# Kernel tuning notes

Measured on AMD Instinct MI355X. Metric: run time of the kernel, lower is better.

The kernel has to match this reference:

```python
import jax, jax.numpy as jnp
import numpy as np

DIM = 128  # matches init kwarg `dim`; scale = 1/sqrt(dim)


def setup_inputs() -> dict:
    key = jax.random.key(0)
    kq, kk, kv = jax.random.split(key, 3)
    B, S, D = 16, 2048, 128
    return {
        "query": jax.random.normal(kq, (B, S, D), dtype=jnp.float32),
        "key": jax.random.normal(kk, (B, S, D), dtype=jnp.float32),
        "value": jax.random.normal(kv, (B, S, D), dtype=jnp.float32),
    }


def reference(query, key, value):
    # scores = Q K^T / sqrt(dim)  -> [B, S, S]
    scale = 1.0 / np.sqrt(DIM).astype(np.float32)
    scores = jnp.einsum("bqd,bkd->bqk", query, key) * scale
    attn = jax.nn.softmax(scores, axis=-1)
    # context = attn @ V -> [B, S, D]
    return jnp.einsum("bqk,bkd->bqd", attn, value)
```

## Files before the change

### kernel.cpp

```cpp
#include <hip/hip_runtime.h>
#include <hip/hip_bf16.h>

namespace {

constexpr int kS  = 2048;
constexpr int kD  = 128;
constexpr int kKB = 64;
constexpr int kNT = kS / kKB;
constexpr int kTileUS = 1024 * 8;
constexpr size_t kImgUShorts = (size_t)16 * 32 * kTileUS;

typedef __attribute__((ext_vector_type(8)))  short bf16x8;
typedef __attribute__((ext_vector_type(16))) float f32x16;
typedef __attribute__((ext_vector_type(4)))  unsigned int u32x4;

__device__ inline unsigned short f2bf(float f) {
  return __builtin_bit_cast(unsigned short, __float2bfloat16(f));
}
__device__ inline unsigned pk2(float lo, float hi) {
  return (unsigned)f2bf(lo) | ((unsigned)f2bf(hi) << 16);
}
__device__ inline float fexp2(float x) { return __builtin_amdgcn_exp2f(x); }

__device__ inline void gload_lds16(const void* g, void* l) {
  __builtin_amdgcn_global_load_lds(
      (const __attribute__((address_space(1))) unsigned int*)g,
      (__attribute__((address_space(3))) unsigned int*)l, 16, 0, 0);
}

__global__ __launch_bounds__(256)
void convert_kv(const float* __restrict__ K, const float* __restrict__ V,
                unsigned short* __restrict__ Kws, unsigned short* __restrict__ Vws)
{
  const int tid = threadIdx.x;
  const int gid = blockIdx.x & 511;
  const int b = gid >> 5, t = gid & 31;
  if (blockIdx.x < 512) {
    const float* src = K + ((size_t)b * kS + t * kKB) * kD;
    unsigned short* dst = Kws + (size_t)gid * kTileUS;
#pragma unroll
    for (int i = 0; i < 4; ++i) {
      const int CH = i * 256 + tid;
      const int k = CH >> 4, s = CH & 15;
      const int d8 = s ^ (k & 15);
      const float* p = src + (size_t)k * kD + d8 * 8;
      float4 a = *reinterpret_cast<const float4*>(p);
      float4 c = *reinterpret_cast<const float4*>(p + 4);
      bf16x8 o;
      o[0] = (short)f2bf(a.x); o[1] = (short)f2bf(a.y);
      o[2] = (short)f2bf(a.z); o[3] = (short)f2bf(a.w);
      o[4] = (short)f2bf(c.x); o[5] = (short)f2bf(c.y);
      o[6] = (short)f2bf(c.z); o[7] = (short)f2bf(c.w);
      *reinterpret_cast<bf16x8*>(dst + (size_t)CH * 8) = o;
    }
  } else {
    __shared__ unsigned short VT[128 * 72];
    const float* src = V + ((size_t)b * kS + t * kKB) * kD;
#pragma unroll
    for (int i = 0; i < 8; ++i) {
      const int idx = i * 256 + tid;
      const int k = idx >> 5, d4 = idx & 31;
      float4 v = *reinterpret_cast<const float4*>(src + (size_t)k * kD + d4 * 4);
      VT[(d4 * 4 + 0) * 72 + k] = f2bf(v.x);
      VT[(d4 * 4 + 1) * 72 + k] = f2bf(v.y);
      VT[(d4 * 4 + 2) * 72 + k] = f2bf(v.z);
      VT[(d4 * 4 + 3) * 72 + k] = f2bf(v.w);
    }
    __syncthreads();
    unsigned short* dst = Vws + (size_t)gid * kTileUS;
#pragma unroll
    for (int i = 0; i < 4; ++i) {
      const int CH = i * 256 + tid;
      const int d = CH >> 3, s = CH & 7;
      const int k8 = s ^ (d & 7);
      bf16x8 v = *reinterpret_cast<const bf16x8*>(&VT[d * 72 + k8 * 8]);
      *reinterpret_cast<bf16x8*>(dst + (size_t)CH * 8) = v;
    }
  }
}

__global__ __launch_bounds__(256, 2)
void attn_fwd(const float* __restrict__ Q,
              const unsigned short* __restrict__ Kws,
              const unsigned short* __restrict__ Vws,
              float* __restrict__ O)
{
  __shared__ __align__(16) unsigned char smem[65536];
  __shared__ float mls[2 * 2 * 32];

  const int tid  = threadIdx.x;
  const int wv   = tid >> 6;
  const int qg   = wv >> 1;
  const int ksp  = wv & 1;
  const int lane = tid & 63;
  const int l31  = lane & 31;
  const int hi   = lane >> 5;
  const int m15  = l31 & 15;
  const int m7   = l31 & 7;

  const int bid   = blockIdx.x;
  const int xcd   = bid & 7;
  const int slot  = bid >> 3;
  const int batch = xcd * 2 + (slot >> 5);
  const int qt    = slot & 31;

  const float* Qb = Q + (size_t)batch * kS * kD;
  float*       Ob = O + (size_t)batch * kS * kD;
  const int qrow0 = qt * 64 + qg * 32;

  auto stageK = [&](int t, int buf) {
    const unsigned short* src = Kws + (size_t)(batch * 32 + t) * kTileUS + (wv * 256 + lane) * 8;
    unsigned char* kd = smem + buf * 16384 + wv * 4096;
    gload_lds16(src,            kd);
    gload_lds16(src + 64 * 8,   kd + 1024);
    gload_lds16(src + 128 * 8,  kd + 2048);
    gload_lds16(src + 192 * 8,  kd + 3072);
  };
  auto stageV = [&](int t, int buf) {
    const unsigned short* src = Vws + (size_t)(batch * 32 + t) * kTileUS + (wv * 256 + lane) * 8;
    unsigned char* vd = smem + 32768 + buf * 16384 + wv * 4096;
    gload_lds16(src,            vd);
    gload_lds16(src + 64 * 8,   vd + 1024);
    gload_lds16(src + 128 * 8,  vd + 2048);
    gload_lds16(src + 192 * 8,  vd + 3072);
  };

  stageK(0, 0); stageV(0, 0); stageK(1, 1);

  constexpr float kQScale = 0.08838834764831845f * 1.4426950408889634f;
  bf16x8 qf[8];
#pragma unroll
  for (int c = 0; c < 8; ++c) {
    const float* p = Qb + (size_t)(qrow0 + l31) * kD + c * 16 + hi * 8;
    float4 a = *reinterpret_cast<const float4*>(p);
    float4 b = *reinterpret_cast<const float4*>(p + 4);
    bf16x8 f;
    f[0] = (short)f2bf(a.x * kQScale); f[1] = (short)f2bf(a.y * kQScale);
    f[2] = (short)f2bf(a.z * kQScale); f[3] = (short)f2bf(a.w * kQScale);
    f[4] = (short)f2bf(b.x * kQScale); f[5] = (short)f2bf(b.y * kQScale);
    f[6] = (short)f2bf(b.z * kQScale); f[7] = (short)f2bf(b.w * kQScale);
    qf[c] = f;
  }

  f32x16 acc[4];
#pragma unroll
  for (int dt = 0; dt < 4; ++dt)
#pragma unroll
    for (int r = 0; r < 16; ++r) acc[dt][r] = 0.f;
  float mrun = -1e30f, lrun = 0.f;
  bf16x8 pa0, pa1;

  __syncthreads();

  const unsigned short* Ksm = reinterpret_cast<const unsigned short*>(smem);
  const unsigned short* Vsm = reinterpret_cast<const unsigned short*>(smem + 32768);
  const int kRowBase = (ksp * 32 + l31) * 128;

  auto qk = [&](int kb) -> f32x16 {
    f32x16 sc;
#pragma unroll
    for (int r = 0; r < 16; ++r) sc[r] = 0.f;
    __builtin_amdgcn_s_setprio(1);
#pragma unroll
    for (int c = 0; c < 8; ++c) {
      const int s = ((c << 1) | hi) ^ m15;
      bf16x8 kf = *reinterpret_cast<const bf16x8*>(&Ksm[kb * 8192 + kRowBase + s * 8]);
      sc = __builtin_amdgcn_mfma_f32_32x32x16_bf16(kf, qf[c], sc, 0, 0, 0);
    }
    __builtin_amdgcn_s_setprio(0);
    return sc;
  };
  auto treemax = [&](const f32x16& sc) {
    float m0 = sc[0];
#pragma unroll
    for (int r = 1; r < 16; ++r) m0 = fmaxf(m0, sc[r]);
    return fmaxf(m0, __shfl_xor(m0, 32));
  };
  auto pv = [&](int vb) {
    const int o0 = (ksp << 2) | hi;
    __builtin_amdgcn_s_setprio(1);
#pragma unroll
    for (int dt = 0; dt < 4; ++dt) {
      const int vRow = vb * 8192 + (dt * 32 + l31) * 64;
      bf16x8 vf0 = *reinterpret_cast<const bf16x8*>(&Vsm[vRow + (o0 ^ m7) * 8]);
      acc[dt] = __builtin_amdgcn_mfma_f32_32x32x16_bf16(vf0, pa0, acc[dt], 0, 0, 0);
      bf16x8 vf1 = *reinterpret_cast<const bf16x8*>(&Vsm[vRow + ((o0 ^ 2) ^ m7) * 8]);
      acc[dt] = __builtin_amdgcn_mfma_f32_32x32x16_bf16(vf1, pa1, acc[dt], 0, 0, 0);
    }
    __builtin_amdgcn_s_setprio(0);
  };
  auto pack = [&](const f32x16& p) {
    unsigned a0 = pk2(p[0], p[1]),   a1 = pk2(p[2],  p[3]);
    unsigned a2 = pk2(p[4], p[5]),   a3 = pk2(p[6],  p[7]);
    unsigned b0 = pk2(p[8], p[9]),   b1 = pk2(p[10], p[11]);
    unsigned b2 = pk2(p[12], p[13]), b3 = pk2(p[14], p[15]);
    asm("v_permlane32_swap_b32 %0, %1" : "+v"(a0), "+v"(a2));
    asm("v_permlane32_swap_b32 %0, %1" : "+v"(a1), "+v"(a3));
    asm("v_permlane32_swap_b32 %0, %1" : "+v"(b0), "+v"(b2));
    asm("v_permlane32_swap_b32 %0, %1" : "+v"(b1), "+v"(b3));
    u32x4 w0 = {a0, a1, a2, a3};
    u32x4 w1 = {b0, b1, b2, b3};
    pa0 = __builtin_bit_cast(bf16x8, w0);
    pa1 = __builtin_bit_cast(bf16x8, w1);
  };

  {
    f32x16 sc = qk(0);
    mrun = treemax(sc);
    float rs = 0.f;
#pragma unroll
    for (int r = 0; r < 16; ++r) { sc[r] = fexp2(sc[r] - mrun); rs += sc[r]; }
    rs += __shfl_xor(rs, 32);
    lrun = rs;
    pack(sc);
  }
  __syncthreads();

  for (int t = 0; t < kNT - 1; ++t) {
    const int kb = (t + 1) & 1, vb = t & 1;
    if (t + 2 < kNT) stageK(t + 2, vb);
    stageV(t + 1, kb);

    f32x16 sc = qk(kb);
    const float mt = treemax(sc);
    const bool need = !__all(mt - mrun <= 8.0f);
    const float mnew = need ? fmaxf(mrun, mt) : mrun;

    pv(vb);

    float rs = 0.f;
#pragma unroll
    for (int r = 0; r < 16; ++r) { sc[r] = fexp2(sc[r] - mnew); rs += sc[r]; }
    rs += __shfl_xor(rs, 32);
    if (need) {
      const float corr = fexp2(mrun - mnew);
      lrun *= corr;
#pragma unroll
      for (int dt = 0; dt < 4; ++dt)
#pragma unroll
        for (int r = 0; r < 16; ++r) acc[dt][r] *= corr;
    }
    lrun += rs;
    mrun = mnew;
    pack(sc);

    __syncthreads();
  }

  pv((kNT - 1) & 1);
  __syncthreads();

  float* scr = reinterpret_cast<float*>(smem);
  auto scrAt = [&](int reg, int q, int d) -> float& {
    return scr[reg * 4096 + q * 128 + (d ^ ((q & 7) << 2))];
  };
  auto drow = [&](int r) { return (r & 3) + 8 * (r >> 2) + 4 * hi; };

  if (ksp == 1) {
#pragma unroll
    for (int dt = 0; dt < 4; ++dt)
#pragma unroll
      for (int r = 0; r < 16; ++r)
        scrAt(qg, l31, dt * 32 + drow(r)) = acc[dt][r];
    mls[(qg * 2 + 0) * 32 + l31] = mrun;
    mls[(qg * 2 + 1) * 32 + l31] = lrun;
  }
  __syncthreads();
  if (ksp == 0) {
    const float m2 = mls[(qg * 2 + 0) * 32 + l31];
    const float l2 = mls[(qg * 2 + 1) * 32 + l31];
    const float mm = fmaxf(mrun, m2);
    const float w1 = fexp2(mrun - mm), w2 = fexp2(m2 - mm);
    const float inv = 1.0f / (lrun * w1 + l2 * w2);
#pragma unroll
    for (int dt = 0; dt < 4; ++dt)
#pragma unroll
      for (int r = 0; r < 16; ++r) {
        const int d = dt * 32 + drow(r);
        float o1 = scrAt(qg, l31, d);
        scrAt(qg, l31, d) = (acc[dt][r] * w1 + o1 * w2) * inv;
      }
  }
  __syncthreads();
  const int krow = tid >> 5, c4 = tid & 31;
#pragma unroll
  for (int i = 0; i < 8; ++i) {
    const int row = i * 8 + krow;
    const int q = row & 31;
    float4 val = *reinterpret_cast<const float4*>(
        &scr[(row >> 5) * 4096 + q * 128 + ((c4 * 4) ^ ((q & 7) << 2))]);
    *reinterpret_cast<float4*>(&Ob[(size_t)(qt * 64 + row) * kD + c4 * 4]) = val;
  }
}

}

extern "C" void kernel_launch(void* const* d_in, const int* in_sizes, int n_in,
                              void* d_out, int out_size, void* d_ws, size_t ws_size,
                              hipStream_t stream) {
  const float* Q = (const float*)d_in[0];
  const float* K = (const float*)d_in[1];
  const float* V = (const float*)d_in[2];
  float* O = (float*)d_out;
  (void)in_sizes; (void)n_in; (void)out_size; (void)ws_size;

  unsigned short* Kws = (unsigned short*)d_ws;
  unsigned short* Vws = Kws + kImgUShorts;

  hipLaunchKernelGGL(convert_kv, dim3(1024), dim3(256), 0, stream, K, V, Kws, Vws);
  hipLaunchKernelGGL(attn_fwd,   dim3(512),  dim3(256), 0, stream, Q, Kws, Vws, O);
}
```

Baseline: 69.51 us.

## Use 512-thread blocks with 128 query rows and triple-buffered K/V LDS pipeline

Doubles the block to 8 waves covering 128 query rows, so each K/V tile staged into LDS is reused by twice as many queries and global-to-LDS traffic per query is halved. The LDS ring grows to three buffers per operand. Full __syncthreads are replaced by explicit vmcnt waits plus a raw s_barrier, which lets a prefetch stay in flight across iterations. The cost is 96KB of LDS per block, which may limit occupancy to one block per CU, and a grid of only 256 blocks.

```diff
diff --git a/kernel.cpp b/kernel.cpp
--- a/kernel.cpp
+++ b/kernel.cpp
@@ -79,14 +79,14 @@
   }
 }
 
-__global__ __launch_bounds__(256, 2)
+__global__ __launch_bounds__(512, 2)
 void attn_fwd(const float* __restrict__ Q,
               const unsigned short* __restrict__ Kws,
               const unsigned short* __restrict__ Vws,
               float* __restrict__ O)
 {
-  __shared__ __align__(16) unsigned char smem[65536];
-  __shared__ float mls[2 * 2 * 32];
+  __shared__ __align__(16) unsigned char smem[98304];
+  __shared__ float mls[4 * 2 * 32];
 
   const int tid  = threadIdx.x;
   const int wv   = tid >> 6;
@@ -101,31 +101,25 @@
   const int bid   = blockIdx.x;
   const int xcd   = bid & 7;
   const int slot  = bid >> 3;
-  const int batch = xcd * 2 + (slot >> 5);
-  const int qt    = slot & 31;
+  const int batch = xcd * 2 + (slot >> 4);
+  const int qt    = slot & 15;
 
   const float* Qb = Q + (size_t)batch * kS * kD;
   float*       Ob = O + (size_t)batch * kS * kD;
-  const int qrow0 = qt * 64 + qg * 32;
+  const int qrow0 = qt * 128 + qg * 32;
 
   auto stageK = [&](int t, int buf) {
-    const unsigned short* src = Kws + (size_t)(batch * 32 + t) * kTileUS + (wv * 256 + lane) * 8;
-    unsigned char* kd = smem + buf * 16384 + wv * 4096;
-    gload_lds16(src,            kd);
-    gload_lds16(src + 64 * 8,   kd + 1024);
-    gload_lds16(src + 128 * 8,  kd + 2048);
-    gload_lds16(src + 192 * 8,  kd + 3072);
+    const unsigned short* src = Kws + (size_t)(batch * 32 + t) * kTileUS + (wv * 128 + lane) * 8;
+    unsigned char* kd = smem + buf * 16384 + wv * 2048;
+    gload_lds16(src,          kd);
+    gload_lds16(src + 64 * 8, kd + 1024);
   };
   auto stageV = [&](int t, int buf) {
-    const unsigned short* src = Vws + (size_t)(batch * 32 + t) * kTileUS + (wv * 256 + lane) * 8;
-    unsigned char* vd = smem + 32768 + buf * 16384 + wv * 4096;
-    gload_lds16(src,            vd);
-    gload_lds16(src + 64 * 8,   vd + 1024);
-    gload_lds16(src + 128 * 8,  vd + 2048);
-    gload_lds16(src + 192 * 8,  vd + 3072);
-  };
-
-  stageK(0, 0); stageV(0, 0); stageK(1, 1);
+    const unsigned short* src = Vws + (size_t)(batch * 32 + t) * kTileUS + (wv * 128 + lane) * 8;
+    unsigned char* vd = smem + 49152 + buf * 16384 + wv * 2048;
+    gload_lds16(src,          vd);
+    gload_lds16(src + 64 * 8, vd + 1024);
+  };
 
   constexpr float kQScale = 0.08838834764831845f * 1.4426950408889634f;
   bf16x8 qf[8];
@@ -142,6 +136,8 @@
     qf[c] = f;
   }
 
+  stageK(0, 0); stageV(0, 0); stageK(1, 1);
+
   f32x16 acc[4];
 #pragma unroll
   for (int dt = 0; dt < 4; ++dt)
@@ -150,10 +146,8 @@
   float mrun = -1e30f, lrun = 0.f;
   bf16x8 pa0, pa1;
 
-  __syncthreads();
-
   const unsigned short* Ksm = reinterpret_cast<const unsigned short*>(smem);
-  const unsigned short* Vsm = reinterpret_cast<const unsigned short*>(smem + 32768);
+  const unsigned short* Vsm = reinterpret_cast<const unsigned short*>(smem + 49152);
   const int kRowBase = (ksp * 32 + l31) * 128;
 
   auto qk = [&](int kb) -> f32x16 {
@@ -204,6 +198,10 @@
     pa1 = __builtin_bit_cast(bf16x8, w1);
   };
 
+  asm volatile("s_waitcnt vmcnt(4)" ::: "memory");
+  __builtin_amdgcn_sched_barrier(0);
+  __builtin_amdgcn_s_barrier();
+  __builtin_amdgcn_sched_barrier(0);
   {
     f32x16 sc = qk(0);
     mrun = treemax(sc);
@@ -214,19 +212,27 @@
     lrun = rs;
     pack(sc);
   }
-  __syncthreads();
-
+
+  int vRead = 0, kRead = 1, kStage = 2;
   for (int t = 0; t < kNT - 1; ++t) {
-    const int kb = (t + 1) & 1, vb = t & 1;
-    if (t + 2 < kNT) stageK(t + 2, vb);
-    stageV(t + 1, kb);
-
-    f32x16 sc = qk(kb);
+    if (t < kNT - 2) {
+      stageK(t + 2, kStage);
+      stageV(t + 1, kRead);
+      asm volatile("s_waitcnt vmcnt(4)" ::: "memory");
+    } else {
+      stageV(t + 1, kRead);
+      asm volatile("s_waitcnt vmcnt(2)" ::: "memory");
+    }
+    __builtin_amdgcn_sched_barrier(0);
+    __builtin_amdgcn_s_barrier();
+    __builtin_amdgcn_sched_barrier(0);
+
+    f32x16 sc = qk(kRead);
     const float mt = treemax(sc);
     const bool need = !__all(mt - mrun <= 8.0f);
     const float mnew = need ? fmaxf(mrun, mt) : mrun;
 
-    pv(vb);
+    pv(vRead);
 
     float rs = 0.f;
 #pragma unroll
@@ -244,10 +250,14 @@
     mrun = mnew;
     pack(sc);
 
-    __syncthreads();
-  }
-
-  pv((kNT - 1) & 1);
+    vRead = kRead; kRead = kStage; kStage = (kStage == 2) ? 0 : kStage + 1;
+  }
+
+  asm volatile("s_waitcnt vmcnt(0)" ::: "memory");
+  __builtin_amdgcn_sched_barrier(0);
+  __builtin_amdgcn_s_barrier();
+  __builtin_amdgcn_sched_barrier(0);
+  pv(vRead);
   __syncthreads();
 
   float* scr = reinterpret_cast<float*>(smem);
@@ -285,11 +295,11 @@
   const int krow = tid >> 5, c4 = tid & 31;
 #pragma unroll
   for (int i = 0; i < 8; ++i) {
-    const int row = i * 8 + krow;
+    const int row = i * 16 + krow;
     const int q = row & 31;
     float4 val = *reinterpret_cast<const float4*>(
         &scr[(row >> 5) * 4096 + q * 128 + ((c4 * 4) ^ ((q & 7) << 2))]);
-    *reinterpret_cast<float4*>(&Ob[(size_t)(qt * 64 + row) * kD + c4 * 4]) = val;
+    *reinterpret_cast<float4*>(&Ob[(size_t)(qt * 128 + row) * kD + c4 * 4]) = val;
   }
 }
 
@@ -308,5 +318,5 @@
   unsigned short* Vws = Kws + kImgUShorts;
 
   hipLaunchKernelGGL(convert_kv, dim3(1024), dim3(256), 0, stream, K, V, Kws, Vws);
-  hipLaunchKernelGGL(attn_fwd,   dim3(512),  dim3(256), 0, stream, Q, Kws, Vws, O);
-}
+  hipLaunchKernelGGL(attn_fwd,   dim3(256),  dim3(512), 0, stream, Q, Kws, Vws, O);
+}
```

Result: faster. 64.80 us (-6.8%).
